# Performance work log

Hardware: AMD Instinct MI355X
Metric: run time of the kernel (lower is better)

## Reference

```python
import jax, jax.numpy as jnp
import numpy as np

TEMPERATURE = 1.0

def _cauchy_kernel(x, y, temperature):
    # pairwise squared distances via Gram trick: ||x_i - y_j||^2
    sq_x = jnp.sum(x * x, axis=1)  # [n]
    sq_y = jnp.sum(y * y, axis=1)  # [m]
    d2 = sq_x[:, None] + sq_y[None, :] - 2.0 * (x @ y.T)
    d2 = jnp.maximum(d2, 0.0)
    return 1.0 / (1.0 + d2 / temperature)


def setup_inputs() -> dict:
    key = jax.random.key(0)
    k1, k2 = jax.random.split(key)
    features = jax.random.normal(k1, (8192, 128), dtype=jnp.float32)
    labels = jax.random.randint(k2, (8192,), 0, 1000, dtype=jnp.int64)
    return {"features": features, "labels": labels}


def reference(features, labels):
    b = features.shape[0] // 2
    z1 = features[:b]
    z2 = features[b:]
    z11 = _cauchy_kernel(z1, z1, TEMPERATURE)  # [b,b]
    z22 = _cauchy_kernel(z2, z2, TEMPERATURE)  # [b,b]
    z12 = _cauchy_kernel(z1, z2, TEMPERATURE)  # [b,b]

    eye = jnp.eye(b, dtype=z11.dtype)
    # positive term: mean log of matched-pair kernel (diagonal of z12)
    pos = jnp.sum(jnp.log(jnp.diagonal(z12))) / b
    # negative terms: row sums over [z11 - I | z12] and [z12^T | z22 - I]
    n1 = jnp.mean(jnp.log((z11 - eye).sum(axis=1) + z12.sum(axis=1)))
    n2 = jnp.mean(jnp.log(z12.sum(axis=0) + (z22 - eye).sum(axis=1)))
    neg = (n1 + n2) / 2.0
    return -(pos - neg)
```

## Files before the change

kernel.cpp:

```cpp
#include <hip/hip_runtime.h>
#include <math.h>

#define N_TOTAL 8192
#define BHALF   4096
#define KDIM    128

typedef __bf16 bf16x8 __attribute__((ext_vector_type(8)));
typedef __bf16 bf16x2 __attribute__((ext_vector_type(2)));
typedef float  f32x4  __attribute__((ext_vector_type(4)));

#define GLOAD_LDS16(GSRC, LDST)                                                \
    __builtin_amdgcn_global_load_lds(                                          \
        (const __attribute__((address_space(1))) void*)(GSRC),                 \
        (__attribute__((address_space(3))) void*)(LDST), 16, 0, 0)

__global__ __launch_bounds__(256) void k_prep_pos(const float* __restrict__ F,
                                                  __bf16* __restrict__ Fbf,
                                                  float* __restrict__ sq,
                                                  float* __restrict__ T,
                                                  float* __restrict__ out) {
    int t = threadIdx.x;
    int w = t >> 6, l = t & 63;
    int p = blockIdx.x * 4 + w;
    const float2* r1 = (const float2*)(F + (size_t)p * KDIM);
    const float2* r2 = (const float2*)(F + (size_t)(p + BHALF) * KDIM);
    float2 a = r1[l];
    float2 c = r2[l];

    float s1 = fmaf(a.x, a.x, a.y * a.y);
    float s2 = fmaf(c.x, c.x, c.y * c.y);
    float dp = fmaf(a.x, c.x, a.y * c.y);
#pragma unroll
    for (int off = 32; off > 0; off >>= 1) {
        s1 += __shfl_down(s1, off);
        s2 += __shfl_down(s2, off);
        dp += __shfl_down(dp, off);
    }

    bf16x2 pa, pc;
    pa[0] = (__bf16)a.x; pa[1] = (__bf16)a.y;
    pc[0] = (__bf16)c.x; pc[1] = (__bf16)c.y;
    ((bf16x2*)(Fbf + (size_t)p * KDIM))[l] = pa;
    ((bf16x2*)(Fbf + (size_t)(p + BHALF) * KDIM))[l] = pc;

    __shared__ float posRed[4];
    if (l == 0) {
        sq[p] = s1;
        sq[p + BHALF] = s2;
        T[p] = 0.0f;
        T[p + BHALF] = 0.0f;
        float d2 = fmaxf(s1 + s2 - 2.0f * dp, 0.0f);
        posRed[w] = logf(1.0f + d2);
    }
    __syncthreads();
    if (t == 0) {
        float s = posRed[0] + posRed[1] + posRed[2] + posRed[3];
        atomicAdd(out, s / (float)BHALF);
    }
}

__global__ __launch_bounds__(512, 4) void k_pairwise(
        const __bf16* __restrict__ Fbf,
        const float* __restrict__ sq,
        float* __restrict__ T) {
    int b = blockIdx.x;
    int ti = (int)floorf((129.0f - sqrtf(16641.0f - 8.0f * (float)b)) * 0.5f);
    while (ti * (129 - ti) / 2 > b) --ti;
    while ((ti + 1) * (128 - ti) / 2 <= b) ++ti;
    int tj = ti + (b - ti * (129 - ti) / 2);
    int I = ti * 128, J = tj * 128;
    bool diag = (ti == tj);

    __shared__ __align__(16) __bf16 As[128 * 128];
    __shared__ __align__(16) __bf16 Bs[128 * 128];
    __shared__ float rowAcc[128][2];
    __shared__ float colAcc[128][4];

    int t = threadIdx.x;
    int w = t >> 6;
    int l = t & 63;
    int wr = w >> 1, wc = w & 1;
    int low = l & 15, kb = l >> 4;

    const __bf16* FA = Fbf + (size_t)I * KDIM;
    const __bf16* FB = Fbf + (size_t)J * KDIM;
#pragma unroll
    for (int it = 0; it < 4; ++it) {
        int f = it * 512 + t;
        int row = f >> 4;
        int sg = f & 15;
        int g = sg ^ (row & 15);
        GLOAD_LDS16(FA + row * KDIM + g * 8, As + (size_t)f * 8);
        GLOAD_LDS16(FB + row * KDIM + g * 8, Bs + (size_t)f * 8);
    }
    __syncthreads();

    const bf16x8* Asg = (const bf16x8*)As;
    const bf16x8* Bsg = (const bf16x8*)Bs;
    f32x4 acc[2][4] = {};
#pragma unroll
    for (int s = 0; s < 4; ++s) {
        int g = s * 4 + kb;
        bf16x8 aF[2], bF[4];
#pragma unroll
        for (int fr = 0; fr < 2; ++fr) {
            int R = wr * 32 + fr * 16 + low;
            aF[fr] = Asg[R * 16 + (g ^ low)];
        }
#pragma unroll
        for (int fc = 0; fc < 4; ++fc) {
            int C = wc * 64 + fc * 16 + low;
            bF[fc] = Bsg[C * 16 + (g ^ low)];
        }
#pragma unroll
        for (int fr = 0; fr < 2; ++fr)
#pragma unroll
            for (int fc = 0; fc < 4; ++fc)
                acc[fr][fc] = __builtin_amdgcn_mfma_f32_16x16x32_bf16(
                    aF[fr], bF[fc], acc[fr][fc], 0, 0, 0);
    }

    float sqi[2][4], sqj[4];
#pragma unroll
    for (int fr = 0; fr < 2; ++fr)
#pragma unroll
        for (int r = 0; r < 4; ++r)
            sqi[fr][r] = sq[I + wr * 32 + fr * 16 + kb * 4 + r];
#pragma unroll
    for (int fc = 0; fc < 4; ++fc)
        sqj[fc] = sq[J + wc * 64 + fc * 16 + low];

    float rowPart[2][4] = {};
    float colPart[4] = {0.f, 0.f, 0.f, 0.f};
#pragma unroll
    for (int fr = 0; fr < 2; ++fr) {
#pragma unroll
        for (int fc = 0; fc < 4; ++fc) {
#pragma unroll
            for (int r = 0; r < 4; ++r) {
                float d2 = sqi[fr][r] + sqj[fc] - 2.0f * acc[fr][fc][r];
                d2 = fmaxf(d2, 0.0f);
                float v = __builtin_amdgcn_rcpf(1.0f + d2);
                rowPart[fr][r] += v;
                colPart[fc] += v;
            }
        }
    }

#pragma unroll
    for (int fr = 0; fr < 2; ++fr)
#pragma unroll
        for (int r = 0; r < 4; ++r) {
            float x = rowPart[fr][r];
            x += __shfl_xor(x, 1);
            x += __shfl_xor(x, 2);
            x += __shfl_xor(x, 4);
            x += __shfl_xor(x, 8);
            if (low == 0)
                rowAcc[wr * 32 + fr * 16 + kb * 4 + r][wc] = x;
        }

#pragma unroll
    for (int fc = 0; fc < 4; ++fc) {
        float x = colPart[fc];
        x += __shfl_xor(x, 16);
        x += __shfl_xor(x, 32);
        if (kb == 0)
            colAcc[wc * 64 + fc * 16 + low][wr] = x;
    }
    __syncthreads();

    if (t < 128) {
        atomicAdd(&T[I + t], rowAcc[t][0] + rowAcc[t][1]);
    } else if (t < 256 && !diag) {
        int c = t - 128;
        atomicAdd(&T[J + c],
                  colAcc[c][0] + colAcc[c][1] + colAcc[c][2] + colAcc[c][3]);
    }
}

__global__ __launch_bounds__(256) void k_final(const float* __restrict__ T,
                                               float* __restrict__ out) {
    int t = threadIdx.x;
    int i = blockIdx.x * 256 + t;
    float s = logf(T[i] - 1.0f);
#pragma unroll
    for (int off = 32; off > 0; off >>= 1) s += __shfl_down(s, off);
    __shared__ float red[4];
    int w = t >> 6, l = t & 63;
    if (l == 0) red[w] = s;
    __syncthreads();
    if (t == 0) {
        float S = red[0] + red[1] + red[2] + red[3];
        atomicAdd(out, S / (2.0f * (float)BHALF));
    }
}

extern "C" void kernel_launch(void* const* d_in, const int* in_sizes, int n_in,
                              void* d_out, int out_size, void* d_ws, size_t ws_size,
                              hipStream_t stream) {
    const float* F = (const float*)d_in[0];
    float* out = (float*)d_out;

    char* ws = (char*)d_ws;
    __bf16* Fbf = (__bf16*)ws;
    float*  sq  = (float*)(ws + (size_t)N_TOTAL * KDIM * 2);
    float*  T   = sq + N_TOTAL;

    hipMemsetAsync(out, 0, sizeof(float), stream);

    k_prep_pos<<<BHALF / 4, 256, 0, stream>>>(F, Fbf, sq, T, out);

    int nTiles = N_TOTAL / 128;
    int nBlocks = nTiles * (nTiles + 1) / 2;
    k_pairwise<<<nBlocks, 512, 0, stream>>>(Fbf, sq, T);

    k_final<<<N_TOTAL / 256, 256, 0, stream>>>(T, out);
}
```

Before: 98.39 us.

## Fuse final reduction into pairwise kernel via last-block ticket counter

Removes the separate final-reduction kernel and the output memset. The last pairwise block to finish, detected with an atomic ticket counter, computes the log-sum over the row totals and the positive-pair partials, then writes the scalar directly. This saves a kernel launch and a memset in exchange for an extra block-wide sync, a fence and an atomic in every pairwise block, plus a serial 8192-element tail done by a single block.

Measured after the change: 145.7 us. 48.0% more time.

```diff
diff --git a/kernel.cpp b/kernel.cpp
--- a/kernel.cpp
+++ b/kernel.cpp
@@ -4,6 +4,8 @@
 #define N_TOTAL 8192
 #define BHALF   4096
 #define KDIM    128
+#define NTILES  64
+#define NBLK    (NTILES * (NTILES + 1) / 2)
 
 typedef __bf16 bf16x8 __attribute__((ext_vector_type(8)));
 typedef __bf16 bf16x2 __attribute__((ext_vector_type(2)));
@@ -18,7 +20,8 @@
                                                   __bf16* __restrict__ Fbf,
                                                   float* __restrict__ sq,
                                                   float* __restrict__ T,
-                                                  float* __restrict__ out) {
+                                                  float* __restrict__ posPart,
+                                                  unsigned int* __restrict__ cnt) {
     int t = threadIdx.x;
     int w = t >> 6, l = t & 63;
     int p = blockIdx.x * 4 + w;
@@ -54,15 +57,18 @@
     }
     __syncthreads();
     if (t == 0) {
-        float s = posRed[0] + posRed[1] + posRed[2] + posRed[3];
-        atomicAdd(out, s / (float)BHALF);
+        posPart[blockIdx.x] = posRed[0] + posRed[1] + posRed[2] + posRed[3];
+        if (blockIdx.x == 0) *cnt = 0u;
     }
 }
 
 __global__ __launch_bounds__(512, 4) void k_pairwise(
         const __bf16* __restrict__ Fbf,
         const float* __restrict__ sq,
-        float* __restrict__ T) {
+        float* __restrict__ T,
+        const float* __restrict__ posPart,
+        unsigned int* __restrict__ cnt,
+        float* __restrict__ out) {
     int b = blockIdx.x;
     int ti = (int)floorf((129.0f - sqrtf(16641.0f - 8.0f * (float)b)) * 0.5f);
     while (ti * (129 - ti) / 2 > b) --ti;
@@ -75,6 +81,8 @@
     __shared__ __align__(16) __bf16 Bs[128 * 128];
     __shared__ float rowAcc[128][2];
     __shared__ float colAcc[128][4];
+    __shared__ float finRed[8];
+    __shared__ unsigned int ticket;
 
     int t = threadIdx.x;
     int w = t >> 6;
@@ -177,22 +185,33 @@
         atomicAdd(&T[J + c],
                   colAcc[c][0] + colAcc[c][1] + colAcc[c][2] + colAcc[c][3]);
     }
-}
-
-__global__ __launch_bounds__(256) void k_final(const float* __restrict__ T,
-                                               float* __restrict__ out) {
-    int t = threadIdx.x;
-    int i = blockIdx.x * 256 + t;
-    float s = logf(T[i] - 1.0f);
+    __syncthreads();
+
+    if (t == 0) {
+        __threadfence();
+        ticket = __hip_atomic_fetch_add(cnt, 1u, __ATOMIC_ACQ_REL,
+                                        __HIP_MEMORY_SCOPE_AGENT);
+    }
+    __syncthreads();
+    if (ticket != (unsigned int)(NBLK - 1)) return;
+
+    float s = 0.0f;
+    for (int i = t; i < N_TOTAL; i += 512) {
+        float Ti = __hip_atomic_load(&T[i], __ATOMIC_RELAXED,
+                                     __HIP_MEMORY_SCOPE_AGENT);
+        s += logf(Ti - 1.0f);
+    }
+    s *= 0.5f;
+    for (int i = t; i < 1024; i += 512) s += posPart[i];
 #pragma unroll
     for (int off = 32; off > 0; off >>= 1) s += __shfl_down(s, off);
-    __shared__ float red[4];
-    int w = t >> 6, l = t & 63;
-    if (l == 0) red[w] = s;
+    if (l == 0) finRed[w] = s;
     __syncthreads();
     if (t == 0) {
-        float S = red[0] + red[1] + red[2] + red[3];
-        atomicAdd(out, S / (2.0f * (float)BHALF));
+        float S = 0.0f;
+#pragma unroll
+        for (int i = 0; i < 8; ++i) S += finRed[i];
+        out[0] = S / (float)BHALF;
     }
 }
 
@@ -203,17 +222,12 @@
     float* out = (float*)d_out;
 
     char* ws = (char*)d_ws;
-    __bf16* Fbf = (__bf16*)ws;
-    float*  sq  = (float*)(ws + (size_t)N_TOTAL * KDIM * 2);
-    float*  T   = sq + N_TOTAL;
-
-    hipMemsetAsync(out, 0, sizeof(float), stream);
-
-    k_prep_pos<<<BHALF / 4, 256, 0, stream>>>(F, Fbf, sq, T, out);
-
-    int nTiles = N_TOTAL / 128;
-    int nBlocks = nTiles * (nTiles + 1) / 2;
-    k_pairwise<<<nBlocks, 512, 0, stream>>>(Fbf, sq, T);
-
-    k_final<<<N_TOTAL / 256, 256, 0, stream>>>(T, out);
+    __bf16* Fbf     = (__bf16*)ws;
+    float*  sq      = (float*)(ws + (size_t)N_TOTAL * KDIM * 2);
+    float*  T       = sq + N_TOTAL;
+    float*  posPart = T + N_TOTAL;
+    unsigned int* cnt = (unsigned int*)(posPart + 1024);
+
+    k_prep_pos<<<BHALF / 4, 256, 0, stream>>>(F, Fbf, sq, T, posPart, cnt);
+    k_pairwise<<<NBLK, 512, 0, stream>>>(Fbf, sq, T, posPart, cnt, out);
 }
```
